# Kernel tuning notes

Hardware: AMD Instinct MI355X
Metric: run time of the kernel (lower is better)

## Reference

```python
import jax, jax.numpy as jnp
import numpy as np

BS, C_IN, NP, NA = 2, 64, 1024, 60
NA_OUT, KS, ANN = 60, 3, 8
C_OUT = 128


def setup_inputs() -> dict:
    key = jax.random.key(0)
    k1, k2, k3, k4 = jax.random.split(key, 4)
    feats = jax.random.normal(k1, (BS, C_IN, NP, NA), dtype=jnp.float32)
    # precomputed anchor-neighbor weights, normalized over the ann axis
    w = jax.random.uniform(k2, (NA_OUT, KS, ANN), dtype=jnp.float32)
    intra_w = w / jnp.sum(w, axis=-1, keepdims=True)
    intra_idx = jax.random.randint(k3, (NA_OUT, KS, ANN), 0, NA)
    # xavier-normal-ish weight for the basic conv, flattened [C_OUT, C_IN*KS]
    W = jax.random.normal(k4, (C_OUT, C_IN * KS), dtype=jnp.float32) * (2.0 / np.sqrt(C_IN * KS + C_OUT))
    bias = jnp.full((1, C_OUT, 1), 0.001, dtype=jnp.float32)
    return {"feats": feats, "intra_w": intra_w, "W": W, "bias": bias, "intra_idx": intra_idx}


def reference(feats, intra_w, W, bias, intra_idx):
    bs, c, npts, na = feats.shape
    na_out, ks, ann = intra_idx.shape
    dim_out = W.shape[0]
    # intra_zpconv_grouping_naive: gather over anchor axis then weighted sum over ann
    g = feats[:, :, :, intra_idx]                      # [b, c, p, o, k, a]
    grouped = jnp.einsum('bcpoka,oka->bckpo', g, intra_w)  # [b, c, ks, p, na_out]
    # BasicZPConv: view to [b, c*ks, p*na_out], W @ x + bias
    x = grouped.reshape(bs, c * ks, npts * na_out)
    out = jnp.einsum('oi,bin->bon', W, x) + bias       # [b, dim_out, p*na_out]
    return out.reshape(bs, dim_out, npts, na_out)
```

## Files before the change

kernel.cpp:

```cpp
#include <hip/hip_runtime.h>

#define NPTS 1024
#define NA   60
#define CIN  64
#define KSZ  3
#define ANN  8
#define COUT 128
#define KD   192

using bf16x8 = __attribute__((ext_vector_type(8))) short;
using f32x4  = __attribute__((ext_vector_type(4))) float;

__device__ __forceinline__ unsigned short f2bf(float f) {
    unsigned int u = __builtin_bit_cast(unsigned int, f);
    u += 0x7FFFu + ((u >> 16) & 1u);
    return (unsigned short)(u >> 16);
}

__global__ void build_tables(const float* __restrict__ intra_w,
                             const float* __restrict__ W,
                             const int*   __restrict__ intra_idx,
                             unsigned short* __restrict__ ws) {
    int f = blockIdx.x * 256 + threadIdx.x;
    if (f < 24576) {
        int j = f & 7, l = (f >> 3) & 63, x = f >> 9;
        int kt = x % 6, mt = x / 6;
        int m  = mt * 16 + (l & 15);
        int ip = kt * 32 + 8 * (l >> 4) + j;
        int c  = ip & 63, ks = ip >> 6;
        ws[f] = f2bf(W[m * KD + c * KSZ + ks]);
    } else if (f < 36864) {
        int f2 = f - 24576;
        int j = f2 & 7, l = (f2 >> 3) & 63;
        int kt = (f2 >> 9) & 1, nt = f2 >> 10;
        int np = nt * 16 + (l & 15);
        int ap = kt * 32 + 8 * (l >> 4) + j;
        float s = 0.f;
        if (np < 180 && ap < 60) {
            int ks = (np >= 120) ? 2 : ((np >= 60) ? 1 : 0);
            int o  = np - 60 * ks;
            const int*   ix = intra_idx + (o * KSZ + ks) * ANN;
            const float* wx = intra_w   + (o * KSZ + ks) * ANN;
            #pragma unroll
            for (int a = 0; a < ANN; a++) s += (ix[a] == ap) ? wx[a] : 0.f;
        }
        ws[f] = f2bf(s);
    }
}

__global__ __launch_bounds__(256, 4)
void intrazp_mfma(const float* __restrict__ feats,
                  const float* __restrict__ bias,
                  const unsigned short* __restrict__ ws,
                  float* __restrict__ out) {
    __shared__ __align__(16) unsigned short fsS[64 * 64];
    __shared__ __align__(16) unsigned short AsT[64 * 192];

    const int t    = threadIdx.x;
    const int wave = t >> 6, lane = t & 63;
    const int l15  = lane & 15, g = lane >> 4;
    const int bid = blockIdx.x;
    const int bp  = (bid & 7) * 256 + (bid >> 3);
    const int b   = bp >> 10, p = bp & 1023;

    {
        const float* fb = feats + (size_t)b * CIN * NPTS * NA + (size_t)p * NA;
        #pragma unroll
        for (int r = 0; r < 4; r++) {
            int q = t + r * 256;
            if (q < 960) {
                int c = q / 15, w = q - c * 15;
                float4 v = *(const float4*)(fb + (size_t)c * NPTS * NA + w * 4);
                unsigned int lo = (unsigned int)f2bf(v.x) | ((unsigned int)f2bf(v.y) << 16);
                unsigned int hi = (unsigned int)f2bf(v.z) | ((unsigned int)f2bf(v.w) << 16);
                int byte = (c * 128 + w * 8) ^ ((c & 7) << 4);
                *(uint2*)((char*)fsS + byte) = make_uint2(lo, hi);
            }
        }
        if (t < 64) {
            int byte = (t * 128 + 120) ^ ((t & 7) << 4);
            *(uint2*)((char*)fsS + byte) = make_uint2(0u, 0u);
        }
        if (t < 192) {
            *(uint2*)((char*)AsT + 60 * 384 + t * 8) = make_uint2(0u, 0u);
        }
    }
    __syncthreads();

    const unsigned short* Sfrag = ws + 24576;
    const int wm = wave & 1, wn = wave >> 1;

    bf16x8 a1[2][2];
    #pragma unroll
    for (int mi = 0; mi < 2; mi++) {
        int c = (2 * wm + mi) * 16 + l15;
        #pragma unroll
        for (int kt = 0; kt < 2; kt++) {
            int byte = (c * 128 + kt * 64 + g * 16) ^ ((c & 7) << 4);
            a1[mi][kt] = *(const bf16x8*)((char*)fsS + byte);
        }
    }

    #pragma unroll
    for (int ni = 0; ni < 6; ni++) {
        int nt = wn * 6 + ni;
        bf16x8 b0 = *(const bf16x8*)(Sfrag + ((nt * 2 + 0) * 64 + lane) * 8);
        bf16x8 b1 = *(const bf16x8*)(Sfrag + ((nt * 2 + 1) * 64 + lane) * 8);

        int np = nt * 16 + l15;
        int ks = (np >= 120) ? 2 : ((np >= 60) ? 1 : 0);
        int o  = np - 60 * ks;
        int sw = (o & 7) << 4;
        int rowbyte = o * 384;

        #pragma unroll
        for (int mi = 0; mi < 2; mi++) {
            f32x4 acc = {0.f, 0.f, 0.f, 0.f};
            acc = __builtin_amdgcn_mfma_f32_16x16x32_bf16(a1[mi][0], b0, acc, 0, 0, 0);
            acc = __builtin_amdgcn_mfma_f32_16x16x32_bf16(a1[mi][1], b1, acc, 0, 0, 0);
            if (np < 180) {
                int cbase = (2 * wm + mi) * 16 + 4 * g;
                int ipb   = ks * 64 + cbase;
                unsigned int lo = (unsigned int)f2bf(acc[0]) | ((unsigned int)f2bf(acc[1]) << 16);
                unsigned int hi = (unsigned int)f2bf(acc[2]) | ((unsigned int)f2bf(acc[3]) << 16);
                int byte = (rowbyte + ipb * 2) ^ sw;
                *(uint2*)((char*)AsT + byte) = make_uint2(lo, hi);
            }
        }
    }

    bf16x8 a2[2][6];
    #pragma unroll
    for (int mi = 0; mi < 2; mi++)
        #pragma unroll
        for (int kt = 0; kt < 6; kt++)
            a2[mi][kt] = *(const bf16x8*)(ws + (((wave * 2 + mi) * 6 + kt) * 64 + lane) * 8);

    __syncthreads();

    int rb[4], swz[4], ov[4];
    #pragma unroll
    for (int nt = 0; nt < 4; nt++) {
        int o = nt * 16 + l15;
        ov[nt]  = o;
        rb[nt]  = o * 384;
        swz[nt] = (o & 7) << 4;
    }

    f32x4 acc[2][4];
    #pragma unroll
    for (int mi = 0; mi < 2; mi++)
        #pragma unroll
        for (int nt = 0; nt < 4; nt++) acc[mi][nt] = (f32x4){0.f, 0.f, 0.f, 0.f};

    #pragma unroll
    for (int kt = 0; kt < 6; kt++) {
        int x = (kt * 32 + 8 * g) * 2;
        bf16x8 bb[4];
        #pragma unroll
        for (int nt = 0; nt < 4; nt++)
            bb[nt] = *(const bf16x8*)((char*)AsT + ((rb[nt] + x) ^ swz[nt]));
        #pragma unroll
        for (int mi = 0; mi < 2; mi++)
            #pragma unroll
            for (int nt = 0; nt < 4; nt++)
                acc[mi][nt] = __builtin_amdgcn_mfma_f32_16x16x32_bf16(a2[mi][kt], bb[nt], acc[mi][nt], 0, 0, 0);
    }

    #pragma unroll
    for (int mi = 0; mi < 2; mi++) {
        int cbase = (wave * 2 + mi) * 16 + 4 * g;
        float bv0 = bias[cbase + 0], bv1 = bias[cbase + 1];
        float bv2 = bias[cbase + 2], bv3 = bias[cbase + 3];
        float* ob = out + (((size_t)b * COUT + cbase) * NPTS + p) * NA;
        const size_t cs = (size_t)NPTS * NA;
        #pragma unroll
        for (int nt = 0; nt < 4; nt++) {
            if (ov[nt] < NA) {
                ob[0 * cs + ov[nt]] = acc[mi][nt][0] + bv0;
                ob[1 * cs + ov[nt]] = acc[mi][nt][1] + bv1;
                ob[2 * cs + ov[nt]] = acc[mi][nt][2] + bv2;
                ob[3 * cs + ov[nt]] = acc[mi][nt][3] + bv3;
            }
        }
    }
}

extern "C" void kernel_launch(void* const* d_in, const int* in_sizes, int n_in,
                              void* d_out, int out_size, void* d_ws, size_t ws_size,
                              hipStream_t stream) {
    const float* feats     = (const float*)d_in[0];
    const float* intra_w   = (const float*)d_in[1];
    const float* W         = (const float*)d_in[2];
    const float* bias      = (const float*)d_in[3];
    const int*   intra_idx = (const int*)d_in[4];
    float* out = (float*)d_out;
    unsigned short* ws = (unsigned short*)d_ws;

    build_tables<<<dim3(144), dim3(256), 0, stream>>>(intra_w, W, intra_idx, ws);
    intrazp_mfma<<<dim3(2 * NPTS), dim3(256), 0, stream>>>(feats, bias, ws, out);
}
```

Measured before the change: 117.9 us.

## Split fused gather+conv kernel into gather kernel and separate conv kernel

Splits the single fused kernel into two. The first does the anchor gather via MFMA and writes the bf16 intermediate to global workspace in MFMA fragment order. The second runs the 128x192 weight GEMM with one point per wave, which gives each wave more accumulators and reloads W fragments from global memory. This adds roughly 50MB of extra global traffic (about 25MB written, then read back) and an extra launch, in exchange for a different occupancy and register balance in each kernel.

```diff
diff --git a/kernel.cpp b/kernel.cpp
--- a/kernel.cpp
+++ b/kernel.cpp
@@ -16,6 +16,7 @@
     u += 0x7FFFu + ((u >> 16) & 1u);
     return (unsigned short)(u >> 16);
 }
+
 
 __global__ void build_tables(const float* __restrict__ intra_w,
                              const float* __restrict__ W,
@@ -49,19 +50,17 @@
 }
 
 __global__ __launch_bounds__(256, 4)
-void intrazp_mfma(const float* __restrict__ feats,
-                  const float* __restrict__ bias,
-                  const unsigned short* __restrict__ ws,
-                  float* __restrict__ out) {
+void intrazp_gather(const float* __restrict__ feats,
+                    unsigned short* __restrict__ ws) {
     __shared__ __align__(16) unsigned short fsS[64 * 64];
     __shared__ __align__(16) unsigned short AsT[64 * 192];
 
     const int t    = threadIdx.x;
     const int wave = t >> 6, lane = t & 63;
     const int l15  = lane & 15, g = lane >> 4;
-    const int bid = blockIdx.x;
-    const int bp  = (bid & 7) * 256 + (bid >> 3);
-    const int b   = bp >> 10, p = bp & 1023;
+    const int bid  = blockIdx.x;
+    const int bp   = (bid & 7) * 256 + (bid >> 3);
+    const int b    = bp >> 10, p = bp & 1023;
 
     {
         const float* fb = feats + (size_t)b * CIN * NPTS * NA + (size_t)p * NA;
@@ -129,58 +128,70 @@
         }
     }
 
-    bf16x8 a2[2][6];
-    #pragma unroll
-    for (int mi = 0; mi < 2; mi++)
-        #pragma unroll
-        for (int kt = 0; kt < 6; kt++)
-            a2[mi][kt] = *(const bf16x8*)(ws + (((wave * 2 + mi) * 6 + kt) * 64 + lane) * 8);
-
     __syncthreads();
 
-    int rb[4], swz[4], ov[4];
-    #pragma unroll
-    for (int nt = 0; nt < 4; nt++) {
-        int o = nt * 16 + l15;
-        ov[nt]  = o;
-        rb[nt]  = o * 384;
-        swz[nt] = (o & 7) << 4;
-    }
-
-    f32x4 acc[2][4];
-    #pragma unroll
-    for (int mi = 0; mi < 2; mi++)
-        #pragma unroll
-        for (int nt = 0; nt < 4; nt++) acc[mi][nt] = (f32x4){0.f, 0.f, 0.f, 0.f};
+    unsigned short* AsD = ws + 36864 + (size_t)bp * 12288;
+    #pragma unroll
+    for (int r = 0; r < 6; r++) {
+        int q  = t + r * 256;
+        int l  = q & 63, ntkt = q >> 6;
+        int nt = ntkt & 3, kt = ntkt >> 2;
+        int o  = nt * 16 + (l & 15);
+        int col = kt * 32 + 8 * (l >> 4);
+        int byte = (o * 384 + col * 2) ^ ((o & 7) << 4);
+        *(bf16x8*)(AsD + (size_t)q * 8) = *(const bf16x8*)((char*)AsT + byte);
+    }
+}
+
+__global__ __launch_bounds__(256, 2)
+void intrazp_conv(const unsigned short* __restrict__ ws,
+                  const float* __restrict__ bias,
+                  float* __restrict__ out) {
+    const int t    = threadIdx.x;
+    const int wave = t >> 6, lane = t & 63;
+    const int l15  = lane & 15, g = lane >> 4;
+    const int bid  = blockIdx.x;
+    const int blk  = (bid & 7) * 64 + (bid >> 3);
+    const int bp   = blk * 4 + wave;
+    const int b    = bp >> 10, p = bp & 1023;
+
+    const unsigned short* Bf = ws + 36864 + (size_t)bp * 12288;
+
+    f32x4 acc[8][4];
+    #pragma unroll
+    for (int mt = 0; mt < 8; mt++)
+        #pragma unroll
+        for (int nt = 0; nt < 4; nt++) acc[mt][nt] = (f32x4){0.f, 0.f, 0.f, 0.f};
 
     #pragma unroll
     for (int kt = 0; kt < 6; kt++) {
-        int x = (kt * 32 + 8 * g) * 2;
         bf16x8 bb[4];
         #pragma unroll
         for (int nt = 0; nt < 4; nt++)
-            bb[nt] = *(const bf16x8*)((char*)AsT + ((rb[nt] + x) ^ swz[nt]));
-        #pragma unroll
-        for (int mi = 0; mi < 2; mi++)
+            bb[nt] = *(const bf16x8*)(Bf + ((size_t)(kt * 4 + nt) * 64 + lane) * 8);
+        #pragma unroll
+        for (int mt = 0; mt < 8; mt++) {
+            bf16x8 a2 = *(const bf16x8*)(ws + ((size_t)(mt * 6 + kt) * 64 + lane) * 8);
             #pragma unroll
             for (int nt = 0; nt < 4; nt++)
-                acc[mi][nt] = __builtin_amdgcn_mfma_f32_16x16x32_bf16(a2[mi][kt], bb[nt], acc[mi][nt], 0, 0, 0);
-    }
-
-    #pragma unroll
-    for (int mi = 0; mi < 2; mi++) {
-        int cbase = (wave * 2 + mi) * 16 + 4 * g;
-        float bv0 = bias[cbase + 0], bv1 = bias[cbase + 1];
-        float bv2 = bias[cbase + 2], bv3 = bias[cbase + 3];
+                acc[mt][nt] = __builtin_amdgcn_mfma_f32_16x16x32_bf16(a2, bb[nt], acc[mt][nt], 0, 0, 0);
+        }
+    }
+
+    #pragma unroll
+    for (int mt = 0; mt < 8; mt++) {
+        int cbase = mt * 16 + 4 * g;
+        float4 bv = *(const float4*)(bias + cbase);
         float* ob = out + (((size_t)b * COUT + cbase) * NPTS + p) * NA;
         const size_t cs = (size_t)NPTS * NA;
         #pragma unroll
         for (int nt = 0; nt < 4; nt++) {
-            if (ov[nt] < NA) {
-                ob[0 * cs + ov[nt]] = acc[mi][nt][0] + bv0;
-                ob[1 * cs + ov[nt]] = acc[mi][nt][1] + bv1;
-                ob[2 * cs + ov[nt]] = acc[mi][nt][2] + bv2;
-                ob[3 * cs + ov[nt]] = acc[mi][nt][3] + bv3;
+            int o = nt * 16 + l15;
+            if (o < NA) {
+                ob[0 * cs + o] = acc[mt][nt][0] + bv.x;
+                ob[1 * cs + o] = acc[mt][nt][1] + bv.y;
+                ob[2 * cs + o] = acc[mt][nt][2] + bv.z;
+                ob[3 * cs + o] = acc[mt][nt][3] + bv.w;
             }
         }
     }
@@ -198,5 +209,6 @@
     unsigned short* ws = (unsigned short*)d_ws;
 
     build_tables<<<dim3(144), dim3(256), 0, stream>>>(intra_w, W, intra_idx, ws);
-    intrazp_mfma<<<dim3(2 * NPTS), dim3(256), 0, stream>>>(feats, bias, ws, out);
-}
+    intrazp_gather<<<dim3(2 * NPTS), dim3(256), 0, stream>>>(feats, ws);
+    intrazp_conv<<<dim3(512), dim3(256), 0, stream>>>(ws, bias, out);
+}
```

Result: slower. 129.7 us (+10.0%).

## Process eight points per block with register-resident weight tables

Applied to the files above, without the earlier changes.

Each block now has 512 threads and handles 8 consecutive points instead of one, so the grid drops from 2048 blocks to 256. All 8 points' features are staged into shared memory in one load. The selection and conv weight fragments are loaded into registers once per block and reused across the points. This amortizes the global table loads and the launch overhead. In exchange, the per-point work runs serially with two barriers per iteration, and each block uses more registers and LDS. On a GPU with many CUs, 256 blocks may also give low occupancy and leave load and compute overlapping less.

```diff
diff --git a/kernel.cpp b/kernel.cpp
--- a/kernel.cpp
+++ b/kernel.cpp
@@ -48,38 +48,60 @@
     }
 }
 
-__global__ __launch_bounds__(256, 4)
-void intrazp_mfma(const float* __restrict__ feats,
-                  const float* __restrict__ bias,
-                  const unsigned short* __restrict__ ws,
-                  float* __restrict__ out) {
-    __shared__ __align__(16) unsigned short fsS[64 * 64];
+__global__ __launch_bounds__(512, 2)
+void intrazp_persist(const float* __restrict__ feats,
+                     const float* __restrict__ bias,
+                     const unsigned short* __restrict__ ws,
+                     float* __restrict__ out) {
+    __shared__ __align__(16) unsigned short fsS2[64 * 8 * 64];
     __shared__ __align__(16) unsigned short AsT[64 * 192];
 
     const int t    = threadIdx.x;
     const int wave = t >> 6, lane = t & 63;
     const int l15  = lane & 15, g = lane >> 4;
-    const int bid = blockIdx.x;
-    const int bp  = (bid & 7) * 256 + (bid >> 3);
-    const int b   = bp >> 10, p = bp & 1023;
+    const int x    = blockIdx.x;
+    const int b    = x >> 7, pbase = (x & 127) * 8;
+
+    const int wm  = wave & 1, wn = wave >> 1;
+    const int h   = wave >> 2, nt2 = wave & 3;
+
+    const unsigned short* Sfrag = ws + 24576;
+    bf16x8 Sreg[3][2];
+    #pragma unroll
+    for (int ni = 0; ni < 3; ni++)
+        #pragma unroll
+        for (int kt = 0; kt < 2; kt++)
+            Sreg[ni][kt] = *(const bf16x8*)(Sfrag + (((3 * wn + ni) * 2 + kt) * 64 + lane) * 8);
+
+    bf16x8 Wreg[4][6];
+    #pragma unroll
+    for (int m = 0; m < 4; m++)
+        #pragma unroll
+        for (int kt = 0; kt < 6; kt++)
+            Wreg[m][kt] = *(const bf16x8*)(ws + (((h * 4 + m) * 6 + kt) * 64 + lane) * 8);
+
+    float4 bvv[4];
+    #pragma unroll
+    for (int m = 0; m < 4; m++)
+        bvv[m] = *(const float4*)(bias + (h * 4 + m) * 16 + 4 * g);
 
     {
-        const float* fb = feats + (size_t)b * CIN * NPTS * NA + (size_t)p * NA;
+        const float* fb = feats + (size_t)b * CIN * NPTS * NA + (size_t)pbase * NA;
         #pragma unroll
-        for (int r = 0; r < 4; r++) {
-            int q = t + r * 256;
-            if (q < 960) {
-                int c = q / 15, w = q - c * 15;
-                float4 v = *(const float4*)(fb + (size_t)c * NPTS * NA + w * 4);
-                unsigned int lo = (unsigned int)f2bf(v.x) | ((unsigned int)f2bf(v.y) << 16);
-                unsigned int hi = (unsigned int)f2bf(v.z) | ((unsigned int)f2bf(v.w) << 16);
-                int byte = (c * 128 + w * 8) ^ ((c & 7) << 4);
-                *(uint2*)((char*)fsS + byte) = make_uint2(lo, hi);
-            }
+        for (int r = 0; r < 15; r++) {
+            int gid = r * 512 + t;
+            int c  = gid / 120, u = gid - c * 120;
+            int pt = u / 15,   w = u - pt * 15;
+            float4 v = *(const float4*)(fb + (size_t)c * NPTS * NA + pt * NA + w * 4);
+            unsigned int lo = (unsigned int)f2bf(v.x) | ((unsigned int)f2bf(v.y) << 16);
+            unsigned int hi = (unsigned int)f2bf(v.z) | ((unsigned int)f2bf(v.w) << 16);
+            int byte = (c * 1024 + pt * 128 + w * 8) ^ ((c & 7) << 4);
+            *(uint2*)((char*)fsS2 + byte) = make_uint2(lo, hi);
         }
-        if (t < 64) {
-            int byte = (t * 128 + 120) ^ ((t & 7) << 4);
-            *(uint2*)((char*)fsS + byte) = make_uint2(0u, 0u);
+        {
+            int c = t >> 3, pt = t & 7;
+            int byte = (c * 1024 + pt * 128 + 120) ^ ((c & 7) << 4);
+            *(uint2*)((char*)fsS2 + byte) = make_uint2(0u, 0u);
         }
         if (t < 192) {
             *(uint2*)((char*)AsT + 60 * 384 + t * 8) = make_uint2(0u, 0u);
@@ -87,102 +109,74 @@
     }
     __syncthreads();
 
-    const unsigned short* Sfrag = ws + 24576;
-    const int wm = wave & 1, wn = wave >> 1;
-
-    bf16x8 a1[2][2];
-    #pragma unroll
-    for (int mi = 0; mi < 2; mi++) {
-        int c = (2 * wm + mi) * 16 + l15;
-        #pragma unroll
-        for (int kt = 0; kt < 2; kt++) {
-            int byte = (c * 128 + kt * 64 + g * 16) ^ ((c & 7) << 4);
-            a1[mi][kt] = *(const bf16x8*)((char*)fsS + byte);
-        }
-    }
-
-    #pragma unroll
-    for (int ni = 0; ni < 6; ni++) {
-        int nt = wn * 6 + ni;
-        bf16x8 b0 = *(const bf16x8*)(Sfrag + ((nt * 2 + 0) * 64 + lane) * 8);
-        bf16x8 b1 = *(const bf16x8*)(Sfrag + ((nt * 2 + 1) * 64 + lane) * 8);
-
-        int np = nt * 16 + l15;
-        int ks = (np >= 120) ? 2 : ((np >= 60) ? 1 : 0);
-        int o  = np - 60 * ks;
-        int sw = (o & 7) << 4;
-        int rowbyte = o * 384;
-
+    for (int pt = 0; pt < 8; ++pt) {
+        bf16x8 a1[2][2];
         #pragma unroll
         for (int mi = 0; mi < 2; mi++) {
-            f32x4 acc = {0.f, 0.f, 0.f, 0.f};
-            acc = __builtin_amdgcn_mfma_f32_16x16x32_bf16(a1[mi][0], b0, acc, 0, 0, 0);
-            acc = __builtin_amdgcn_mfma_f32_16x16x32_bf16(a1[mi][1], b1, acc, 0, 0, 0);
-            if (np < 180) {
-                int cbase = (2 * wm + mi) * 16 + 4 * g;
-                int ipb   = ks * 64 + cbase;
-                unsigned int lo = (unsigned int)f2bf(acc[0]) | ((unsigned int)f2bf(acc[1]) << 16);
-                unsigned int hi = (unsigned int)f2bf(acc[2]) | ((unsigned int)f2bf(acc[3]) << 16);
-                int byte = (rowbyte + ipb * 2) ^ sw;
-                *(uint2*)((char*)AsT + byte) = make_uint2(lo, hi);
+            int c = (wm * 2 + mi) * 16 + l15;
+            #pragma unroll
+            for (int kt = 0; kt < 2; kt++) {
+                int byte = (c * 1024 + pt * 128 + kt * 64 + g * 16) ^ ((c & 7) << 4);
+                a1[mi][kt] = *(const bf16x8*)((char*)fsS2 + byte);
             }
         }
-    }
+        #pragma unroll
+        for (int ni = 0; ni < 3; ni++) {
+            int nt = 3 * wn + ni;
+            int np = nt * 16 + l15;
+            int ks = (np >= 120) ? 2 : ((np >= 60) ? 1 : 0);
+            int o  = np - 60 * ks;
+            int sw = (o & 7) << 4;
+            int rowbyte = o * 384;
+            #pragma unroll
+            for (int mi = 0; mi < 2; mi++) {
+                f32x4 acc1 = {0.f, 0.f, 0.f, 0.f};
+                acc1 = __builtin_amdgcn_mfma_f32_16x16x32_bf16(a1[mi][0], Sreg[ni][0], acc1, 0, 0, 0);
+                acc1 = __builtin_amdgcn_mfma_f32_16x16x32_bf16(a1[mi][1], Sreg[ni][1], acc1, 0, 0, 0);
+                if (np < 180) {
+                    int cbase = (wm * 2 + mi) * 16 + 4 * g;
+                    int ipb   = ks * 64 + cbase;
+                    unsigned int lo = (unsigned int)f2bf(acc1[0]) | ((unsigned int)f2bf(acc1[1]) << 16);
+                    unsigned int hi = (unsigned int)f2bf(acc1[2]) | ((unsigned int)f2bf(acc1[3]) << 16);
+                    int byte = (rowbyte + ipb * 2) ^ sw;
+                    *(uint2*)((char*)AsT + byte) = make_uint2(lo, hi);
+                }
+            }
+        }
 
-    bf16x8 a2[2][6];
-    #pragma unroll
-    for (int mi = 0; mi < 2; mi++)
+        __syncthreads();
+
+        int o   = nt2 * 16 + l15;
+        int swo = (o & 7) << 4, rbo = o * 384;
+        bf16x8 bb[6];
         #pragma unroll
         for (int kt = 0; kt < 6; kt++)
-            a2[mi][kt] = *(const bf16x8*)(ws + (((wave * 2 + mi) * 6 + kt) * 64 + lane) * 8);
+            bb[kt] = *(const bf16x8*)((char*)AsT + ((rbo + (kt * 32 + 8 * g) * 2) ^ swo));
 
-    __syncthreads();
+        f32x4 acc[4];
+        #pragma unroll
+        for (int m = 0; m < 4; m++) acc[m] = (f32x4){0.f, 0.f, 0.f, 0.f};
+        #pragma unroll
+        for (int kt = 0; kt < 6; kt++)
+            #pragma unroll
+            for (int m = 0; m < 4; m++)
+                acc[m] = __builtin_amdgcn_mfma_f32_16x16x32_bf16(Wreg[m][kt], bb[kt], acc[m], 0, 0, 0);
 
-    int rb[4], swz[4], ov[4];
-    #pragma unroll
-    for (int nt = 0; nt < 4; nt++) {
-        int o = nt * 16 + l15;
-        ov[nt]  = o;
-        rb[nt]  = o * 384;
-        swz[nt] = (o & 7) << 4;
-    }
-
-    f32x4 acc[2][4];
-    #pragma unroll
-    for (int mi = 0; mi < 2; mi++)
-        #pragma unroll
-        for (int nt = 0; nt < 4; nt++) acc[mi][nt] = (f32x4){0.f, 0.f, 0.f, 0.f};
-
-    #pragma unroll
-    for (int kt = 0; kt < 6; kt++) {
-        int x = (kt * 32 + 8 * g) * 2;
-        bf16x8 bb[4];
-        #pragma unroll
-        for (int nt = 0; nt < 4; nt++)
-            bb[nt] = *(const bf16x8*)((char*)AsT + ((rb[nt] + x) ^ swz[nt]));
-        #pragma unroll
-        for (int mi = 0; mi < 2; mi++)
+        int p = pbase + pt;
+        if (o < NA) {
+            const size_t cs = (size_t)NPTS * NA;
             #pragma unroll
-            for (int nt = 0; nt < 4; nt++)
-                acc[mi][nt] = __builtin_amdgcn_mfma_f32_16x16x32_bf16(a2[mi][kt], bb[nt], acc[mi][nt], 0, 0, 0);
-    }
-
-    #pragma unroll
-    for (int mi = 0; mi < 2; mi++) {
-        int cbase = (wave * 2 + mi) * 16 + 4 * g;
-        float bv0 = bias[cbase + 0], bv1 = bias[cbase + 1];
-        float bv2 = bias[cbase + 2], bv3 = bias[cbase + 3];
-        float* ob = out + (((size_t)b * COUT + cbase) * NPTS + p) * NA;
-        const size_t cs = (size_t)NPTS * NA;
-        #pragma unroll
-        for (int nt = 0; nt < 4; nt++) {
-            if (ov[nt] < NA) {
-                ob[0 * cs + ov[nt]] = acc[mi][nt][0] + bv0;
-                ob[1 * cs + ov[nt]] = acc[mi][nt][1] + bv1;
-                ob[2 * cs + ov[nt]] = acc[mi][nt][2] + bv2;
-                ob[3 * cs + ov[nt]] = acc[mi][nt][3] + bv3;
+            for (int m = 0; m < 4; m++) {
+                int cbase = (h * 4 + m) * 16 + 4 * g;
+                float* ob = out + (((size_t)b * COUT + cbase) * NPTS + p) * NA + o;
+                ob[0 * cs] = acc[m][0] + bvv[m].x;
+                ob[1 * cs] = acc[m][1] + bvv[m].y;
+                ob[2 * cs] = acc[m][2] + bvv[m].z;
+                ob[3 * cs] = acc[m][3] + bvv[m].w;
             }
         }
+
+        __syncthreads();
     }
 }
 
@@ -198,5 +192,5 @@
     unsigned short* ws = (unsigned short*)d_ws;
 
     build_tables<<<dim3(144), dim3(256), 0, stream>>>(intra_w, W, intra_idx, ws);
-    intrazp_mfma<<<dim3(2 * NPTS), dim3(256), 0, stream>>>(feats, bias, ws, out);
+    intrazp_persist<<<dim3(256), dim3(512), 0, stream>>>(feats, bias, ws, out);
 }
```

Result: faster. 105.2 us (-10.8%).

## Process four points per block with register-resident weight fragments

Applied to the files above, without the earlier changes.

Each block now handles four consecutive points instead of one, launching 512 blocks instead of 2048. The grouping matrix fragments, the conv weight fragments and the bias are loaded into registers once per block and reused across the four points. The feature tile for all four points is staged in LDS in a single pass. The cost is higher register pressure (launch bounds lowered to 2 blocks per SM), a serial per-point loop with extra barriers, and fewer blocks to hide latency.

```diff
diff --git a/kernel.cpp b/kernel.cpp
--- a/kernel.cpp
+++ b/kernel.cpp
@@ -48,38 +48,59 @@
     }
 }
 
-__global__ __launch_bounds__(256, 4)
-void intrazp_mfma(const float* __restrict__ feats,
-                  const float* __restrict__ bias,
-                  const unsigned short* __restrict__ ws,
-                  float* __restrict__ out) {
-    __shared__ __align__(16) unsigned short fsS[64 * 64];
+__global__ __launch_bounds__(256, 2)
+void intrazp_persist(const float* __restrict__ feats,
+                     const float* __restrict__ bias,
+                     const unsigned short* __restrict__ ws,
+                     float* __restrict__ out) {
+    __shared__ __align__(16) unsigned short fsS2[64 * 4 * 64];
     __shared__ __align__(16) unsigned short AsT[64 * 192];
 
     const int t    = threadIdx.x;
     const int wave = t >> 6, lane = t & 63;
     const int l15  = lane & 15, g = lane >> 4;
-    const int bid = blockIdx.x;
-    const int bp  = (bid & 7) * 256 + (bid >> 3);
-    const int b   = bp >> 10, p = bp & 1023;
+    const int x    = blockIdx.x;
+    const int b    = x >> 8, pbase = (x & 255) * 4;
+
+    const int wm = wave & 1, wn = wave >> 1;
+
+    const unsigned short* Sfrag = ws + 24576;
+    bf16x8 Sreg[6][2];
+    #pragma unroll
+    for (int ni = 0; ni < 6; ni++)
+        #pragma unroll
+        for (int kt = 0; kt < 2; kt++)
+            Sreg[ni][kt] = *(const bf16x8*)(Sfrag + (((wn * 6 + ni) * 2 + kt) * 64 + lane) * 8);
+
+    bf16x8 Wreg[2][6];
+    #pragma unroll
+    for (int mi = 0; mi < 2; mi++)
+        #pragma unroll
+        for (int kt = 0; kt < 6; kt++)
+            Wreg[mi][kt] = *(const bf16x8*)(ws + (((wave * 2 + mi) * 6 + kt) * 64 + lane) * 8);
+
+    float4 bvv[2];
+    #pragma unroll
+    for (int mi = 0; mi < 2; mi++)
+        bvv[mi] = *(const float4*)(bias + (wave * 2 + mi) * 16 + 4 * g);
 
     {
-        const float* fb = feats + (size_t)b * CIN * NPTS * NA + (size_t)p * NA;
-        #pragma unroll
-        for (int r = 0; r < 4; r++) {
-            int q = t + r * 256;
-            if (q < 960) {
-                int c = q / 15, w = q - c * 15;
-                float4 v = *(const float4*)(fb + (size_t)c * NPTS * NA + w * 4);
-                unsigned int lo = (unsigned int)f2bf(v.x) | ((unsigned int)f2bf(v.y) << 16);
-                unsigned int hi = (unsigned int)f2bf(v.z) | ((unsigned int)f2bf(v.w) << 16);
-                int byte = (c * 128 + w * 8) ^ ((c & 7) << 4);
-                *(uint2*)((char*)fsS + byte) = make_uint2(lo, hi);
-            }
-        }
-        if (t < 64) {
-            int byte = (t * 128 + 120) ^ ((t & 7) << 4);
-            *(uint2*)((char*)fsS + byte) = make_uint2(0u, 0u);
+        const float* fb = feats + (size_t)b * CIN * NPTS * NA + (size_t)pbase * NA;
+        #pragma unroll
+        for (int r = 0; r < 15; r++) {
+            int gid = r * 256 + t;
+            int c  = gid / 60, u = gid - c * 60;
+            int pt = u / 15,   w = u - pt * 15;
+            float4 v = *(const float4*)(fb + (size_t)c * NPTS * NA + pt * NA + w * 4);
+            unsigned int lo = (unsigned int)f2bf(v.x) | ((unsigned int)f2bf(v.y) << 16);
+            unsigned int hi = (unsigned int)f2bf(v.z) | ((unsigned int)f2bf(v.w) << 16);
+            int byte = (c * 512 + pt * 128 + w * 8) ^ ((c & 7) << 4);
+            *(uint2*)((char*)fsS2 + byte) = make_uint2(lo, hi);
+        }
+        {
+            int c = t >> 2, pt = t & 3;
+            int byte = (c * 512 + pt * 128 + 120) ^ ((c & 7) << 4);
+            *(uint2*)((char*)fsS2 + byte) = make_uint2(0u, 0u);
         }
         if (t < 192) {
             *(uint2*)((char*)AsT + 60 * 384 + t * 8) = make_uint2(0u, 0u);
@@ -87,102 +108,90 @@
     }
     __syncthreads();
 
-    const unsigned short* Sfrag = ws + 24576;
-    const int wm = wave & 1, wn = wave >> 1;
-
-    bf16x8 a1[2][2];
-    #pragma unroll
-    for (int mi = 0; mi < 2; mi++) {
-        int c = (2 * wm + mi) * 16 + l15;
-        #pragma unroll
-        for (int kt = 0; kt < 2; kt++) {
-            int byte = (c * 128 + kt * 64 + g * 16) ^ ((c & 7) << 4);
-            a1[mi][kt] = *(const bf16x8*)((char*)fsS + byte);
-        }
-    }
-
-    #pragma unroll
-    for (int ni = 0; ni < 6; ni++) {
-        int nt = wn * 6 + ni;
-        bf16x8 b0 = *(const bf16x8*)(Sfrag + ((nt * 2 + 0) * 64 + lane) * 8);
-        bf16x8 b1 = *(const bf16x8*)(Sfrag + ((nt * 2 + 1) * 64 + lane) * 8);
-
-        int np = nt * 16 + l15;
-        int ks = (np >= 120) ? 2 : ((np >= 60) ? 1 : 0);
-        int o  = np - 60 * ks;
-        int sw = (o & 7) << 4;
-        int rowbyte = o * 384;
-
+    for (int pt = 0; pt < 4; ++pt) {
+        bf16x8 a1[2][2];
         #pragma unroll
         for (int mi = 0; mi < 2; mi++) {
-            f32x4 acc = {0.f, 0.f, 0.f, 0.f};
-            acc = __builtin_amdgcn_mfma_f32_16x16x32_bf16(a1[mi][0], b0, acc, 0, 0, 0);
-            acc = __builtin_amdgcn_mfma_f32_16x16x32_bf16(a1[mi][1], b1, acc, 0, 0, 0);
-            if (np < 180) {
-                int cbase = (2 * wm + mi) * 16 + 4 * g;
-                int ipb   = ks * 64 + cbase;
-                unsigned int lo = (unsigned int)f2bf(acc[0]) | ((unsigned int)f2bf(acc[1]) << 16);
-                unsigned int hi = (unsigned int)f2bf(acc[2]) | ((unsigned int)f2bf(acc[3]) << 16);
-                int byte = (rowbyte + ipb * 2) ^ sw;
-                *(uint2*)((char*)AsT + byte) = make_uint2(lo, hi);
+            int c = (wm * 2 + mi) * 16 + l15;
+            #pragma unroll
+            for (int kt = 0; kt < 2; kt++) {
+                int byte = (c * 512 + pt * 128 + kt * 64 + g * 16) ^ ((c & 7) << 4);
+                a1[mi][kt] = *(const bf16x8*)((char*)fsS2 + byte);
             }
         }
-    }
-
-    bf16x8 a2[2][6];
-    #pragma unroll
-    for (int mi = 0; mi < 2; mi++)
-        #pragma unroll
-        for (int kt = 0; kt < 6; kt++)
-            a2[mi][kt] = *(const bf16x8*)(ws + (((wave * 2 + mi) * 6 + kt) * 64 + lane) * 8);
-
-    __syncthreads();
-
-    int rb[4], swz[4], ov[4];
-    #pragma unroll
-    for (int nt = 0; nt < 4; nt++) {
-        int o = nt * 16 + l15;
-        ov[nt]  = o;
-        rb[nt]  = o * 384;
-        swz[nt] = (o & 7) << 4;
-    }
-
-    f32x4 acc[2][4];
-    #pragma unroll
-    for (int mi = 0; mi < 2; mi++)
-        #pragma unroll
-        for (int nt = 0; nt < 4; nt++) acc[mi][nt] = (f32x4){0.f, 0.f, 0.f, 0.f};
-
-    #pragma unroll
-    for (int kt = 0; kt < 6; kt++) {
-        int x = (kt * 32 + 8 * g) * 2;
-        bf16x8 bb[4];
-        #pragma unroll
-        for (int nt = 0; nt < 4; nt++)
-            bb[nt] = *(const bf16x8*)((char*)AsT + ((rb[nt] + x) ^ swz[nt]));
+        #pragma unroll
+        for (int ni = 0; ni < 6; ni++) {
+            int nt = wn * 6 + ni;
+            int np = nt * 16 + l15;
+            int ks = (np >= 120) ? 2 : ((np >= 60) ? 1 : 0);
+            int o  = np - 60 * ks;
+            int sw = (o & 7) << 4;
+            int rowbyte = o * 384;
+            #pragma unroll
+            for (int mi = 0; mi < 2; mi++) {
+                f32x4 acc1 = {0.f, 0.f, 0.f, 0.f};
+                acc1 = __builtin_amdgcn_mfma_f32_16x16x32_bf16(a1[mi][0], Sreg[ni][0], acc1, 0, 0, 0);
+                acc1 = __builtin_amdgcn_mfma_f32_16x16x32_bf16(a1[mi][1], Sreg[ni][1], acc1, 0, 0, 0);
+                if (np < 180) {
+                    int cbase = (wm * 2 + mi) * 16 + 4 * g;
+                    int ipb   = ks * 64 + cbase;
+                    unsigned int lo = (unsigned int)f2bf(acc1[0]) | ((unsigned int)f2bf(acc1[1]) << 16);
+                    unsigned int hi = (unsigned int)f2bf(acc1[2]) | ((unsigned int)f2bf(acc1[3]) << 16);
+                    int byte = (rowbyte + ipb * 2) ^ sw;
+                    *(uint2*)((char*)AsT + byte) = make_uint2(lo, hi);
+                }
+            }
+        }
+
+        __syncthreads();
+
+        int rb[4], swz[4], ov[4];
+        #pragma unroll
+        for (int nt = 0; nt < 4; nt++) {
+            int o = nt * 16 + l15;
+            ov[nt]  = o;
+            rb[nt]  = o * 384;
+            swz[nt] = (o & 7) << 4;
+        }
+
+        f32x4 acc[2][4];
         #pragma unroll
         for (int mi = 0; mi < 2; mi++)
             #pragma unroll
+            for (int nt = 0; nt < 4; nt++) acc[mi][nt] = (f32x4){0.f, 0.f, 0.f, 0.f};
+
+        #pragma unroll
+        for (int kt = 0; kt < 6; kt++) {
+            int x2 = (kt * 32 + 8 * g) * 2;
+            bf16x8 bb[4];
+            #pragma unroll
             for (int nt = 0; nt < 4; nt++)
-                acc[mi][nt] = __builtin_amdgcn_mfma_f32_16x16x32_bf16(a2[mi][kt], bb[nt], acc[mi][nt], 0, 0, 0);
-    }
-
-    #pragma unroll
-    for (int mi = 0; mi < 2; mi++) {
-        int cbase = (wave * 2 + mi) * 16 + 4 * g;
-        float bv0 = bias[cbase + 0], bv1 = bias[cbase + 1];
-        float bv2 = bias[cbase + 2], bv3 = bias[cbase + 3];
-        float* ob = out + (((size_t)b * COUT + cbase) * NPTS + p) * NA;
-        const size_t cs = (size_t)NPTS * NA;
-        #pragma unroll
-        for (int nt = 0; nt < 4; nt++) {
-            if (ov[nt] < NA) {
-                ob[0 * cs + ov[nt]] = acc[mi][nt][0] + bv0;
-                ob[1 * cs + ov[nt]] = acc[mi][nt][1] + bv1;
-                ob[2 * cs + ov[nt]] = acc[mi][nt][2] + bv2;
-                ob[3 * cs + ov[nt]] = acc[mi][nt][3] + bv3;
+                bb[nt] = *(const bf16x8*)((char*)AsT + ((rb[nt] + x2) ^ swz[nt]));
+            #pragma unroll
+            for (int mi = 0; mi < 2; mi++)
+                #pragma unroll
+                for (int nt = 0; nt < 4; nt++)
+                    acc[mi][nt] = __builtin_amdgcn_mfma_f32_16x16x32_bf16(Wreg[mi][kt], bb[nt], acc[mi][nt], 0, 0, 0);
+        }
+
+        int p = pbase + pt;
+        #pragma unroll
+        for (int mi = 0; mi < 2; mi++) {
+            int cbase = (wave * 2 + mi) * 16 + 4 * g;
+            float* ob = out + (((size_t)b * COUT + cbase) * NPTS + p) * NA;
+            const size_t cs = (size_t)NPTS * NA;
+            #pragma unroll
+            for (int nt = 0; nt < 4; nt++) {
+                if (ov[nt] < NA) {
+                    ob[0 * cs + ov[nt]] = acc[mi][nt][0] + bvv[mi].x;
+                    ob[1 * cs + ov[nt]] = acc[mi][nt][1] + bvv[mi].y;
+                    ob[2 * cs + ov[nt]] = acc[mi][nt][2] + bvv[mi].z;
+                    ob[3 * cs + ov[nt]] = acc[mi][nt][3] + bvv[mi].w;
+                }
             }
         }
+
+        __syncthreads();
     }
 }
 
@@ -198,5 +207,5 @@
     unsigned short* ws = (unsigned short*)d_ws;
 
     build_tables<<<dim3(144), dim3(256), 0, stream>>>(intra_w, W, intra_idx, ws);
-    intrazp_mfma<<<dim3(2 * NPTS), dim3(256), 0, stream>>>(feats, bias, ws, out);
-}
+    intrazp_persist<<<dim3(512), dim3(256), 0, stream>>>(feats, bias, ws, out);
+}
```

New measurement: 106.5 us. 1.11x faster.
